# Kernel optimization log

Hardware: AMD Instinct MI355X
Metric: run time of the kernel (lower is better)

Reference implementation:

```python
import jax, jax.numpy as jnp
import numpy as np
import math

N_HEAD = 16

def setup_inputs() -> dict:
    key = jax.random.key(0)
    ks = jax.random.split(key, 8)
    B, S, P, NX = 4, 1024, 128, 1024
    return {
        "x": jax.random.normal(ks[0], (B, S, NX), jnp.float32),
        "M": jax.random.normal(ks[1], (B, P, NX), jnp.float32),
        "Mmask": jnp.ones((B, P), jnp.float32),
        "attention_mask": jnp.zeros((B, 1, 1, S), jnp.float32),
        "W_attn": jax.random.normal(ks[2], (NX, 3 * NX), jnp.float32) * 0.02,
        "b_attn": jnp.zeros((3 * NX,), jnp.float32),
        "W_mem": jax.random.normal(ks[3], (NX, 2 * NX), jnp.float32) * 0.02,
        "b_mem": jnp.zeros((2 * NX,), jnp.float32),
        "W_proj": jax.random.normal(ks[4], (NX, NX), jnp.float32) * 0.02,
        "b_proj": jnp.zeros((NX,), jnp.float32),
    }

def _split_heads(t, H):
    B, T, NX = t.shape
    return t.reshape(B, T, H, NX // H).transpose(0, 2, 1, 3)  # [B,H,T,dh]

def reference(x, M, Mmask, attention_mask, W_attn, b_attn, W_mem, b_mem, W_proj, b_proj):
    B, S, NX = x.shape
    H = N_HEAD
    dh = NX // H
    P = M.shape[1]

    # fused QKV projection (Conv1D == x @ W + b)
    qkv = x @ W_attn + b_attn
    q, k, v = jnp.split(qkv, 3, axis=2)

    # memory K/V projection, prepended along the key/value sequence axis
    ekv = M @ W_mem + b_mem
    ek, ev = jnp.split(ekv, 2, axis=2)
    key = jnp.concatenate([ek, k], axis=1)   # [B, P+S, NX]
    value = jnp.concatenate([ev, v], axis=1)

    qh = _split_heads(q, H)      # [B,H,S,dh]
    kh = _split_heads(key, H)    # [B,H,P+S,dh]
    vh = _split_heads(value, H)  # [B,H,P+S,dh]

    w = jnp.einsum('bhsd,bhtd->bhst', qh, kh) / math.sqrt(dh)  # [B,H,S,P+S]

    # causal bias over the self part, all-ones over the memory part
    causal = jnp.tril(jnp.ones((S, S), w.dtype))
    b = jnp.concatenate([jnp.ones((S, P), w.dtype), causal], axis=1)[None, None]  # [1,1,S,P+S]
    w = w * b - 10000.0 * (1.0 - b)

    # additive attention mask: memory-mask bias concatenated before token mask
    mem_bias = (1.0 - Mmask)[:, None, None, :] * -10000.0  # [B,1,1,P]
    am = jnp.concatenate([mem_bias, jnp.broadcast_to(attention_mask, (B, 1, 1, S))], axis=3)
    w = w + am

    w = jax.nn.softmax(w, axis=-1)
    a = jnp.einsum('bhst,bhtd->bhsd', w, vh)                  # [B,H,S,dh]
    a = a.transpose(0, 2, 1, 3).reshape(B, S, NX)             # merge heads
    return a @ W_proj + b_proj
```

## Files before the change

### kernel.cpp

```cpp
#include <hip/hip_runtime.h>
#include <hip/hip_bf16.h>


typedef __attribute__((ext_vector_type(8))) short bf16x8;
typedef __attribute__((ext_vector_type(4))) float f32x4;

#define MFMA16(a, b, c) __builtin_amdgcn_mfma_f32_16x16x32_bf16((a), (b), (c), 0, 0, 0)

#define GLOAD_LDS16(g, l)                                                  \
    __builtin_amdgcn_global_load_lds(                                      \
        (const __attribute__((address_space(1))) void*)(const void*)(g),   \
        (__attribute__((address_space(3))) void*)(void*)(l), 16, 0, 0)

static __device__ __forceinline__ unsigned short f2bf(float f) {
    union { float f; unsigned int u; } v; v.f = f;
    unsigned int u = v.u;
    return (unsigned short)((u + 0x7fffu + ((u >> 16) & 1u)) >> 16);
}

static __device__ __forceinline__ void transpose64(const float* __restrict__ W,
                                                   unsigned short* __restrict__ Wt,
                                                   int K, int N, int bx, int by,
                                                   float* tile ) {
    const int n0 = bx * 64, k0 = by * 64;
    const int tr = threadIdx.x >> 2, tc = (threadIdx.x & 3) * 16;
    #pragma unroll
    for (int i = 0; i < 4; i++) {
        float4 v = *(const float4*)&W[(size_t)(k0 + tr) * N + n0 + tc + i * 4];
        tile[tr * 65 + tc + i * 4 + 0] = v.x;
        tile[tr * 65 + tc + i * 4 + 1] = v.y;
        tile[tr * 65 + tc + i * 4 + 2] = v.z;
        tile[tr * 65 + tc + i * 4 + 3] = v.w;
    }
    __syncthreads();
    union { ushort4 u4[2]; unsigned short s[8]; } pk[2];
    #pragma unroll
    for (int half = 0; half < 2; half++)
        #pragma unroll
        for (int i = 0; i < 8; i++)
            pk[half].s[i] = f2bf(tile[(tc + half * 8 + i) * 65 + tr]);
    unsigned short* dst = &Wt[(size_t)(n0 + tr) * K + k0 + tc];
    *(ushort4*)(dst + 0) = pk[0].u4[0];
    *(ushort4*)(dst + 4) = pk[0].u4[1];
    *(ushort4*)(dst + 8) = pk[1].u4[0];
    *(ushort4*)(dst + 12) = pk[1].u4[1];
}

__global__ void prep_all(const float* __restrict__ x, const float* __restrict__ Mem,
                         unsigned short* __restrict__ x_bf, unsigned short* __restrict__ M_bf,
                         const float* __restrict__ W_attn, const float* __restrict__ W_mem,
                         const float* __restrict__ W_proj, unsigned short* __restrict__ Wat,
                         unsigned short* __restrict__ Wmt, unsigned short* __restrict__ Wpt,
                         const float* __restrict__ Mmask, const float* __restrict__ amask,
                         float* __restrict__ biasT) {
    __shared__ float tile[64 * 65];
    int bid = blockIdx.x;
    if (bid < 4608) {
        int i = bid * 256 + threadIdx.x;
        if (i < 1048576) {
            float4 v = ((const float4*)x)[i];
            ushort4 o; o.x = f2bf(v.x); o.y = f2bf(v.y); o.z = f2bf(v.z); o.w = f2bf(v.w);
            ((ushort4*)x_bf)[i] = o;
        } else {
            int j = i - 1048576;
            float4 v = ((const float4*)Mem)[j];
            ushort4 o; o.x = f2bf(v.x); o.y = f2bf(v.y); o.z = f2bf(v.z); o.w = f2bf(v.w);
            ((ushort4*)M_bf)[j] = o;
        }
        return;
    }
    bid -= 4608;
    if (bid < 768) {
        transpose64(W_attn, Wat, 1024, 3072, bid % 48, bid / 48, tile);
    } else if (bid < 1280) {
        int t = bid - 768;  transpose64(W_mem, Wmt, 1024, 2048, t % 32, t / 32, tile);
    } else if (bid < 1536) {
        int t = bid - 1280; transpose64(W_proj, Wpt, 1024, 1024, t % 16, t / 16, tile);
    } else {
        int i = (bid - 1536) * 256 + threadIdx.x;
        if (i < 4 * 1152) {
            int b = i / 1152, t = i % 1152;
            float v = (t < 128) ? (Mmask[b * 128 + t] - 1.f) * 10000.f
                                : amask[b * 1024 + t - 128];
            biasT[i] = v * 1.4426950408889634f;
        }
    }
}

__global__ __launch_bounds__(256, 4) void gemm_fused(
        const unsigned short* __restrict__ x_bf, const unsigned short* __restrict__ Wat,
        const float* __restrict__ b_attn, const unsigned short* __restrict__ M_bf,
        const unsigned short* __restrict__ Wmt, const float* __restrict__ b_mem,
        unsigned short* __restrict__ Qbuf, unsigned short* __restrict__ Kc,
        unsigned short* __restrict__ Vt) {
    __shared__ char smem[34816];
    unsigned short* As = (unsigned short*)smem;
    unsigned short* Bs = (unsigned short*)(smem + 8192);
    const int tid = threadIdx.x;
    const int lane = tid & 63, wave = tid >> 6;
    const int quad = lane >> 4, l16 = lane & 15;
    const int crow = lane >> 2, ccol = (lane & 3) * 8;
    const int bid = blockIdx.x;

    if (bid < 768) {
        const int bm = bid & 31, bn = bid >> 5;
        const int wm = (wave & 1) * 64, wn = (wave >> 1) * 64;
        const unsigned short* Abase = x_bf + (size_t)(bm * 128 + crow) * 1024 + ccol;
        const unsigned short* Bbase = Wat + (size_t)(bn * 128 + crow) * 1024 + ccol;
        f32x4 acc[4][4] = {};
        for (int k0 = 0; k0 < 1024; k0 += 32) {
            __syncthreads();
            #pragma unroll
            for (int cc = 0; cc < 4; cc++) {
                const int c = wave * 4 + cc;
                if (c < 8) GLOAD_LDS16(Abase + (size_t)(c * 16) * 1024 + k0, &As[c * 512]);
                else       GLOAD_LDS16(Bbase + (size_t)((c - 8) * 16) * 1024 + k0, &Bs[(c - 8) * 512]);
            }
            __syncthreads();
            bf16x8 af[4], bf[4];
            #pragma unroll
            for (int i = 0; i < 4; i++) af[i] = *(const bf16x8*)&As[(wm + i * 16 + l16) * 32 + quad * 8];
            #pragma unroll
            for (int j = 0; j < 4; j++) bf[j] = *(const bf16x8*)&Bs[(wn + j * 16 + l16) * 32 + quad * 8];
            #pragma unroll
            for (int i = 0; i < 4; i++)
                #pragma unroll
                for (int j = 0; j < 4; j++)
                    acc[i][j] = MFMA16(af[i], bf[j], acc[i][j]);
        }
        float bj[4];
        #pragma unroll
        for (int j = 0; j < 4; j++) bj[j] = b_attn[bn * 128 + wn + j * 16 + l16];
        __syncthreads();
        if (bn < 8) {
            #pragma unroll
            for (int i = 0; i < 4; i++) {
                const int row = bm * 128 + wm + i * 16 + quad * 4;
                #pragma unroll
                for (int j = 0; j < 4; j++) {
                    const int col = bn * 128 + wn + j * 16 + l16;
                    #pragma unroll
                    for (int r = 0; r < 4; r++)
                        Qbuf[(size_t)(row + r) * 1024 + col] = f2bf(acc[i][j][r] + bj[j]);
                }
            }
        } else if (bn < 16) {
            #pragma unroll
            for (int i = 0; i < 4; i++) {
                const int row = bm * 128 + wm + i * 16 + quad * 4;
                const int b = row >> 10, s = row & 1023;
                #pragma unroll
                for (int j = 0; j < 4; j++) {
                    const int c = bn * 128 + wn + j * 16 + l16 - 1024;
                    unsigned short* kd = Kc + (size_t)((b << 4) | (c >> 6)) * 73728 +
                                         (size_t)(s + 128) * 64 + (c & 63);
                    #pragma unroll
                    for (int r = 0; r < 4; r++) kd[(size_t)r * 64] = f2bf(acc[i][j][r] + bj[j]);
                }
            }
        } else {
            unsigned short* Tw = (unsigned short*)smem + wave * 4352;
            #pragma unroll
            for (int i = 0; i < 4; i++)
                #pragma unroll
                for (int j = 0; j < 4; j++)
                    #pragma unroll
                    for (int r = 0; r < 4; r++)
                        Tw[(j * 16 + l16) * 68 + i * 16 + quad * 4 + r] = f2bf(acc[i][j][r] + bj[j]);
            const int vb = (bn - 16) * 128 + wn;
            const int h = vb >> 6;
            const int b = bm >> 3, s0 = (bm * 128 + wm) & 1023;
            unsigned short* vd = Vt + (size_t)((b << 4) | h) * 73728 +
                                 (size_t)lane * 1152 + 128 + s0;
            #pragma unroll
            for (int ch = 0; ch < 8; ch++)
                *(bf16x8*)(vd + ch * 8) = *(const bf16x8*)&Tw[lane * 68 + ch * 8];
        }
    } else {
        const int t = bid - 768;
        const int bm = t >> 5, bn = t & 31;
        const int wm = (wave & 1) * 32, wn = (wave >> 1) * 32;
        const unsigned short* Abase = M_bf + (size_t)(bm * 64 + crow) * 1024 + ccol;
        const unsigned short* Bbase = Wmt + (size_t)(bn * 64 + crow) * 1024 + ccol;
        f32x4 acc[2][2] = {};
        for (int k0 = 0; k0 < 1024; k0 += 32) {
            __syncthreads();
            #pragma unroll
            for (int cc = 0; cc < 2; cc++) {
                const int c = wave * 2 + cc;
                if (c < 4) GLOAD_LDS16(Abase + (size_t)(c * 16) * 1024 + k0, &As[c * 512]);
                else       GLOAD_LDS16(Bbase + (size_t)((c - 4) * 16) * 1024 + k0, &Bs[(c - 4) * 512]);
            }
            __syncthreads();
            bf16x8 af[2], bf[2];
            #pragma unroll
            for (int i = 0; i < 2; i++) af[i] = *(const bf16x8*)&As[(wm + i * 16 + l16) * 32 + quad * 8];
            #pragma unroll
            for (int j = 0; j < 2; j++) bf[j] = *(const bf16x8*)&Bs[(wn + j * 16 + l16) * 32 + quad * 8];
            #pragma unroll
            for (int i = 0; i < 2; i++)
                #pragma unroll
                for (int j = 0; j < 2; j++)
                    acc[i][j] = MFMA16(af[i], bf[j], acc[i][j]);
        }
        float bj[2];
        #pragma unroll
        for (int j = 0; j < 2; j++) bj[j] = b_mem[bn * 64 + wn + j * 16 + l16];
        __syncthreads();
        if (bn < 16) {
            #pragma unroll
            for (int i = 0; i < 2; i++) {
                const int row = bm * 64 + wm + i * 16 + quad * 4;
                const int b = row >> 7, p = row & 127;
                #pragma unroll
                for (int j = 0; j < 2; j++) {
                    const int c = bn * 64 + wn + j * 16 + l16;
                    unsigned short* kd = Kc + (size_t)((b << 4) | (c >> 6)) * 73728 +
                                         (size_t)p * 64 + (c & 63);
                    #pragma unroll
                    for (int r = 0; r < 4; r++) kd[(size_t)r * 64] = f2bf(acc[i][j][r] + bj[j]);
                }
            }
        } else {
            unsigned short* Tw = (unsigned short*)smem + wave * 1152;
            #pragma unroll
            for (int i = 0; i < 2; i++)
                #pragma unroll
                for (int j = 0; j < 2; j++)
                    #pragma unroll
                    for (int r = 0; r < 4; r++)
                        Tw[(j * 16 + l16) * 36 + i * 16 + quad * 4 + r] = f2bf(acc[i][j][r] + bj[j]);
            const int vb = bn * 64 + wn - 1024;
            const int h = vb >> 6, d0 = vb & 63;
            const int b = (bm * 64 + wm) >> 7, p0 = (bm * 64 + wm) & 127;
            const int lc = lane >> 1, half = lane & 1;
            unsigned short* vd = Vt + (size_t)((b << 4) | h) * 73728 +
                                 (size_t)(d0 + lc) * 1152 + p0 + half * 16;
            #pragma unroll
            for (int ch = 0; ch < 2; ch++)
                *(bf16x8*)(vd + ch * 8) = *(const bf16x8*)&Tw[lc * 36 + half * 16 + ch * 8];
        }
    }
}

__global__ __launch_bounds__(128) void attn_kernel(const unsigned short* __restrict__ Qbuf,
                                                   const unsigned short* __restrict__ Kc,
                                                   const unsigned short* __restrict__ Vt,
                                                   const float* __restrict__ biasT,
                                                   unsigned short* __restrict__ Aout) {
    __shared__ unsigned short Ks[64 * 64];
    __shared__ unsigned short Vs[64 * 64];
    __shared__ unsigned short Ps[2][16 * 72];
    const int tid = threadIdx.x;
    const int lane = tid & 63, wave = tid >> 6;
    const int quad = lane >> 4, l16 = lane & 15;
    const int blk = blockIdx.x;
    const int xcd = blk & 7, idx = blk >> 3;
    const int bh = xcd * 8 + (idx & 7);
    const int pair = idx >> 3;
    const int h = bh & 15, b = bh >> 4;

    const unsigned short* Kb = Kc + (size_t)bh * 73728;
    const unsigned short* Vb = Vt + (size_t)bh * 73728;
    const float* bias_b = biasT + b * 1152;

    const int srow = lane >> 3;
    const int scol = ((lane & 7) ^ srow) * 8;
    const int rswz = l16 & 7;
    const int w32 = wave * 32;

    bf16x8 ones;
    #pragma unroll
    for (int j = 0; j < 8; j++) ones[j] = (short)0x3F80;

    #pragma unroll
    for (int phase = 0; phase < 2; phase++) {
        const int qg = phase ? (31 - pair) : pair;
        const int qrow0 = qg * 32;
        const int qrow_w = qrow0 + wave * 16;

        bf16x8 qf[2];
        #pragma unroll
        for (int k2 = 0; k2 < 2; k2++)
            qf[k2] = *(const bf16x8*)(Qbuf + (size_t)(b * 1024 + qrow_w + l16) * 1024 +
                                      h * 64 + k2 * 32 + quad * 8);

        f32x4 o[4] = {};
        f32x4 oden = {};
        const int tmax = min(1152, ((qrow0 + 223) >> 6) << 6);

        for (int t0 = 0; t0 < tmax; t0 += 64) {
            __syncthreads();
            {
                const unsigned short* gk = Kb + (size_t)(t0 + w32 + srow) * 64 + scol;
                const unsigned short* gv = Vb + (size_t)(w32 + srow) * 1152 + t0 + scol;
                #pragma unroll
                for (int cc = 0; cc < 4; cc++) {
                    GLOAD_LDS16(gk + (size_t)(cc * 8) * 64,   &Ks[(w32 + cc * 8) * 64]);
                    GLOAD_LDS16(gv + (size_t)(cc * 8) * 1152, &Vs[(w32 + cc * 8) * 64]);
                }
            }
            __syncthreads();
            if (t0 <= qrow_w + 143) {
                const bool nomask = (t0 + 63 <= 128 + qrow_w);
                float4 bt[4];
                #pragma unroll
                for (int tn = 0; tn < 4; tn++)
                    bt[tn] = *(const float4*)(bias_b + t0 + tn * 16 + quad * 4);
                const int sg = qrow_w + l16;
                #pragma unroll
                for (int tn = 0; tn < 4; tn++) {
                    bf16x8 kf0 = *(const bf16x8*)&Ks[(tn * 16 + l16) * 64 + (quad ^ rswz) * 8];
                    bf16x8 kf1 = *(const bf16x8*)&Ks[(tn * 16 + l16) * 64 + ((quad + 4) ^ rswz) * 8];
                    f32x4 st = {};
                    st = MFMA16(kf0, qf[0], st);
                    st = MFMA16(kf1, qf[1], st);
                    float p[4];
                    #pragma unroll
                    for (int r = 0; r < 4; r++) {
                        float e = __builtin_amdgcn_exp2f(st[r] * 0.18033688011112042f + bt[tn][r]);
                        if (!nomask) {
                            const int tg = t0 + tn * 16 + quad * 4 + r;
                            e = (tg < 128 || tg - 128 <= sg) ? e : 0.f;
                        }
                        p[r] = e;
                    }
                    union { ushort4 u; __hip_bfloat162 h2[2]; } pk;
                    pk.h2[0] = __float22bfloat162_rn(float2{p[0], p[1]});
                    pk.h2[1] = __float22bfloat162_rn(float2{p[2], p[3]});
                    *(ushort4*)&Ps[wave][l16 * 72 + tn * 16 + quad * 4] = pk.u;
                }
                #pragma unroll
                for (int tk = 0; tk < 2; tk++) {
                    bf16x8 pf = *(const bf16x8*)&Ps[wave][l16 * 72 + tk * 32 + quad * 8];
                    oden = MFMA16(pf, ones, oden);
                    #pragma unroll
                    for (int dn = 0; dn < 4; dn++) {
                        bf16x8 vf = *(const bf16x8*)&Vs[(dn * 16 + l16) * 64 +
                                                        ((tk * 4 + quad) ^ rswz) * 8];
                        o[dn] = MFMA16(pf, vf, o[dn]);
                    }
                }
            }
        }

        #pragma unroll
        for (int r = 0; r < 4; r++) {
            const float inv = 1.f / oden[r];
            const size_t orow = (size_t)(b * 1024 + qrow_w + quad * 4 + r) * 1024 + h * 64;
            #pragma unroll
            for (int dn = 0; dn < 4; dn++)
                Aout[orow + dn * 16 + l16] = f2bf(o[dn][r] * inv);
        }
    }
}

__global__ __launch_bounds__(256) void gemm_proj(const unsigned short* __restrict__ Abuf,
                                                 const unsigned short* __restrict__ Wpt,
                                                 const float* __restrict__ b_proj,
                                                 float* __restrict__ out) {
    __shared__ unsigned short As[128 * 32];
    __shared__ unsigned short Bs[64 * 32];
    const int tid = threadIdx.x;
    const int lane = tid & 63, wave = tid >> 6;
    const int quad = lane >> 4, l16 = lane & 15;
    const int wm = (wave & 1) * 64, wn = (wave >> 1) * 32;
    const int bm = blockIdx.x & 31, bn = blockIdx.x >> 5;
    const int crow = lane >> 2, ccol = (lane & 3) * 8;
    const unsigned short* Abase = Abuf + (size_t)(bm * 128 + crow) * 1024 + ccol;
    const unsigned short* Bbase = Wpt + (size_t)(bn * 64 + crow) * 1024 + ccol;

    f32x4 acc[4][2] = {};
    for (int k0 = 0; k0 < 1024; k0 += 32) {
        __syncthreads();
        #pragma unroll
        for (int cc = 0; cc < 3; cc++) {
            const int c = wave * 3 + cc;
            if (c < 8) GLOAD_LDS16(Abase + (size_t)(c * 16) * 1024 + k0, &As[c * 512]);
            else if (c < 12) GLOAD_LDS16(Bbase + (size_t)((c - 8) * 16) * 1024 + k0, &Bs[(c - 8) * 512]);
        }
        __syncthreads();
        bf16x8 af[4], bf[2];
        #pragma unroll
        for (int i = 0; i < 4; i++) af[i] = *(const bf16x8*)&As[(wm + i * 16 + l16) * 32 + quad * 8];
        #pragma unroll
        for (int j = 0; j < 2; j++) bf[j] = *(const bf16x8*)&Bs[(wn + j * 16 + l16) * 32 + quad * 8];
        #pragma unroll
        for (int i = 0; i < 4; i++)
            #pragma unroll
            for (int j = 0; j < 2; j++)
                acc[i][j] = MFMA16(af[i], bf[j], acc[i][j]);
    }
    float bj[2];
    #pragma unroll
    for (int j = 0; j < 2; j++) bj[j] = b_proj[bn * 64 + wn + j * 16 + l16];
    #pragma unroll
    for (int i = 0; i < 4; i++) {
        const int row = bm * 128 + wm + i * 16 + quad * 4;
        #pragma unroll
        for (int j = 0; j < 2; j++) {
            const int col = bn * 64 + wn + j * 16 + l16;
            #pragma unroll
            for (int r = 0; r < 4; r++)
                out[(size_t)(row + r) * 1024 + col] = acc[i][j][r] + bj[j];
        }
    }
}

extern "C" void kernel_launch(void* const* d_in, const int* in_sizes, int n_in,
                              void* d_out, int out_size, void* d_ws, size_t ws_size,
                              hipStream_t stream) {
    const float* x      = (const float*)d_in[0];
    const float* Mem    = (const float*)d_in[1];
    const float* Mmask  = (const float*)d_in[2];
    const float* amask  = (const float*)d_in[3];
    const float* W_attn = (const float*)d_in[4];
    const float* b_attn = (const float*)d_in[5];
    const float* W_mem  = (const float*)d_in[6];
    const float* b_mem  = (const float*)d_in[7];
    const float* W_proj = (const float*)d_in[8];
    const float* b_proj = (const float*)d_in[9];
    float* out = (float*)d_out;

    char* ws = (char*)d_ws;
    unsigned short* x_bf  = (unsigned short*)ws;  ws += (size_t)4096 * 1024 * 2;
    unsigned short* M_bf  = (unsigned short*)ws;  ws += (size_t)512 * 1024 * 2;
    unsigned short* Wat   = (unsigned short*)ws;  ws += (size_t)3072 * 1024 * 2;
    unsigned short* Wmt   = (unsigned short*)ws;  ws += (size_t)2048 * 1024 * 2;
    unsigned short* Wpt   = (unsigned short*)ws;  ws += (size_t)1024 * 1024 * 2;
    unsigned short* Qbuf  = (unsigned short*)ws;  ws += (size_t)4096 * 1024 * 2;
    unsigned short* Abuf  = (unsigned short*)ws;  ws += (size_t)4096 * 1024 * 2;
    unsigned short* Kc    = (unsigned short*)ws;  ws += (size_t)64 * 1152 * 64 * 2;
    unsigned short* Vt    = (unsigned short*)ws;  ws += (size_t)64 * 64 * 1152 * 2;
    float*          biasT = (float*)ws;           ws += (size_t)4 * 1152 * 4;

    prep_all<<<6163, 256, 0, stream>>>(x, Mem, x_bf, M_bf, W_attn, W_mem, W_proj,
                                       Wat, Wmt, Wpt, Mmask, amask, biasT);
    gemm_fused<<<1024, 256, 0, stream>>>(x_bf, Wat, b_attn, M_bf, Wmt, b_mem,
                                         Qbuf, Kc, Vt);
    attn_kernel<<<1024, 128, 0, stream>>>(Qbuf, Kc, Vt, biasT, Abuf);
    gemm_proj<<<512, 256, 0, stream>>>(Abuf, Wpt, b_proj, out);
}
```

Before: 200.6 us.

## Load K/V fragments directly from global memory, dropping LDS staging and barriers

The attention kernel no longer stages K and V tiles in shared memory through global_load_lds with block-wide barriers. Each wave reads its K and V MFMA fragments straight from global memory and runs its own per-wave loop bound. This removes both __syncthreads per tile and the shared K/V buffers, and it lets waves in a block run out of step. The cost is that both waves now fetch the same K/V data separately through the caches with no prefetch, so global latency lands directly on the MFMA chain.

```diff
diff --git a/kernel.cpp b/kernel.cpp
--- a/kernel.cpp
+++ b/kernel.cpp
@@ -248,8 +248,6 @@
                                                    const unsigned short* __restrict__ Vt,
                                                    const float* __restrict__ biasT,
                                                    unsigned short* __restrict__ Aout) {
-    __shared__ unsigned short Ks[64 * 64];
-    __shared__ unsigned short Vs[64 * 64];
     __shared__ unsigned short Ps[2][16 * 72];
     const int tid = threadIdx.x;
     const int lane = tid & 63, wave = tid >> 6;
@@ -264,11 +262,6 @@
     const unsigned short* Vb = Vt + (size_t)bh * 73728;
     const float* bias_b = biasT + b * 1152;
 
-    const int srow = lane >> 3;
-    const int scol = ((lane & 7) ^ srow) * 8;
-    const int rswz = l16 & 7;
-    const int w32 = wave * 32;
-
     bf16x8 ones;
     #pragma unroll
     for (int j = 0; j < 8; j++) ones[j] = (short)0x3F80;
@@ -287,59 +280,47 @@
 
         f32x4 o[4] = {};
         f32x4 oden = {};
-        const int tmax = min(1152, ((qrow0 + 223) >> 6) << 6);
+        const int tmax = min(1152, (((qrow_w + 143) >> 6) << 6) + 64);
+        const int sg = qrow_w + l16;
 
         for (int t0 = 0; t0 < tmax; t0 += 64) {
-            __syncthreads();
-            {
-                const unsigned short* gk = Kb + (size_t)(t0 + w32 + srow) * 64 + scol;
-                const unsigned short* gv = Vb + (size_t)(w32 + srow) * 1152 + t0 + scol;
-                #pragma unroll
-                for (int cc = 0; cc < 4; cc++) {
-                    GLOAD_LDS16(gk + (size_t)(cc * 8) * 64,   &Ks[(w32 + cc * 8) * 64]);
-                    GLOAD_LDS16(gv + (size_t)(cc * 8) * 1152, &Vs[(w32 + cc * 8) * 64]);
+            const bool nomask = (t0 + 63 <= 128 + qrow_w);
+            float4 bt[4];
+            #pragma unroll
+            for (int tn = 0; tn < 4; tn++)
+                bt[tn] = *(const float4*)(bias_b + t0 + tn * 16 + quad * 4);
+            #pragma unroll
+            for (int tn = 0; tn < 4; tn++) {
+                const unsigned short* krow = Kb + (size_t)(t0 + tn * 16 + l16) * 64 + quad * 8;
+                bf16x8 kf0 = *(const bf16x8*)krow;
+                bf16x8 kf1 = *(const bf16x8*)(krow + 32);
+                f32x4 st = {};
+                st = MFMA16(kf0, qf[0], st);
+                st = MFMA16(kf1, qf[1], st);
+                float p[4];
+                #pragma unroll
+                for (int r = 0; r < 4; r++) {
+                    float e = __builtin_amdgcn_exp2f(st[r] * 0.18033688011112042f + bt[tn][r]);
+                    if (!nomask) {
+                        const int tg = t0 + tn * 16 + quad * 4 + r;
+                        e = (tg < 128 || tg - 128 <= sg) ? e : 0.f;
+                    }
+                    p[r] = e;
                 }
-            }
-            __syncthreads();
-            if (t0 <= qrow_w + 143) {
-                const bool nomask = (t0 + 63 <= 128 + qrow_w);
-                float4 bt[4];
-                #pragma unroll
-                for (int tn = 0; tn < 4; tn++)
-                    bt[tn] = *(const float4*)(bias_b + t0 + tn * 16 + quad * 4);
-                const int sg = qrow_w + l16;
-                #pragma unroll
-                for (int tn = 0; tn < 4; tn++) {
-                    bf16x8 kf0 = *(const bf16x8*)&Ks[(tn * 16 + l16) * 64 + (quad ^ rswz) * 8];
-                    bf16x8 kf1 = *(const bf16x8*)&Ks[(tn * 16 + l16) * 64 + ((quad + 4) ^ rswz) * 8];
-                    f32x4 st = {};
-                    st = MFMA16(kf0, qf[0], st);
-                    st = MFMA16(kf1, qf[1], st);
-                    float p[4];
-                    #pragma unroll
-                    for (int r = 0; r < 4; r++) {
-                        float e = __builtin_amdgcn_exp2f(st[r] * 0.18033688011112042f + bt[tn][r]);
-                        if (!nomask) {
-                            const int tg = t0 + tn * 16 + quad * 4 + r;
-                            e = (tg < 128 || tg - 128 <= sg) ? e : 0.f;
-                        }
-                        p[r] = e;
-                    }
-                    union { ushort4 u; __hip_bfloat162 h2[2]; } pk;
-                    pk.h2[0] = __float22bfloat162_rn(float2{p[0], p[1]});
-                    pk.h2[1] = __float22bfloat162_rn(float2{p[2], p[3]});
-                    *(ushort4*)&Ps[wave][l16 * 72 + tn * 16 + quad * 4] = pk.u;
-                }
-                #pragma unroll
-                for (int tk = 0; tk < 2; tk++) {
-                    bf16x8 pf = *(const bf16x8*)&Ps[wave][l16 * 72 + tk * 32 + quad * 8];
-                    oden = MFMA16(pf, ones, oden);
-                    #pragma unroll
-                    for (int dn = 0; dn < 4; dn++) {
-                        bf16x8 vf = *(const bf16x8*)&Vs[(dn * 16 + l16) * 64 +
-                                                        ((tk * 4 + quad) ^ rswz) * 8];
-                        o[dn] = MFMA16(pf, vf, o[dn]);
-                    }
+                union { ushort4 u; __hip_bfloat162 h2[2]; } pk;
+                pk.h2[0] = __float22bfloat162_rn(float2{p[0], p[1]});
+                pk.h2[1] = __float22bfloat162_rn(float2{p[2], p[3]});
+                *(ushort4*)&Ps[wave][l16 * 72 + tn * 16 + quad * 4] = pk.u;
+            }
+            #pragma unroll
+            for (int tk = 0; tk < 2; tk++) {
+                bf16x8 pf = *(const bf16x8*)&Ps[wave][l16 * 72 + tk * 32 + quad * 8];
+                oden = MFMA16(pf, ones, oden);
+                #pragma unroll
+                for (int dn = 0; dn < 4; dn++) {
+                    bf16x8 vf = *(const bf16x8*)(Vb + (size_t)(dn * 16 + l16) * 1152 +
+                                                 t0 + tk * 32 + quad * 8);
+                    o[dn] = MFMA16(pf, vf, o[dn]);
                 }
             }
         }
```

New measurement: 248.6 us. +23.9%, slower.

## Double-buffer K/V tiles in attention kernel to overlap loads with compute

Applied to the files above, without the earlier changes.

The attention kernel now keeps two LDS buffers for the K and V tiles and issues the global-to-LDS loads for the next tile before computing on the current one. Partial vmcnt waits and raw s_barrier instructions replace the paired __syncthreads, so the next tile's loads stay in flight while the current tile is processed. This doubles the K/V shared-memory footprint, which may reduce occupancy. The hand-counted vmcnt(8) must match the number of outstanding loads for the synchronization to stay correct.

```diff
diff --git a/kernel.cpp b/kernel.cpp
--- a/kernel.cpp
+++ b/kernel.cpp
@@ -248,8 +248,8 @@
                                                    const unsigned short* __restrict__ Vt,
                                                    const float* __restrict__ biasT,
                                                    unsigned short* __restrict__ Aout) {
-    __shared__ unsigned short Ks[64 * 64];
-    __shared__ unsigned short Vs[64 * 64];
+    __shared__ unsigned short Ks[2][64 * 64];
+    __shared__ unsigned short Vs[2][64 * 64];
     __shared__ unsigned short Ps[2][16 * 72];
     const int tid = threadIdx.x;
     const int lane = tid & 63, wave = tid >> 6;
@@ -269,6 +269,17 @@
     const int rswz = l16 & 7;
     const int w32 = wave * 32;
 
+#define STAGE_KV(t0_, kdst_, vdst_)                                            \
+    {                                                                          \
+        const unsigned short* gk = Kb + (size_t)((t0_) + w32 + srow) * 64 + scol; \
+        const unsigned short* gv = Vb + (size_t)(w32 + srow) * 1152 + (t0_) + scol; \
+        _Pragma("unroll")                                                      \
+        for (int cc = 0; cc < 4; cc++) {                                       \
+            GLOAD_LDS16(gk + (size_t)(cc * 8) * 64,   &(kdst_)[(w32 + cc * 8) * 64]); \
+            GLOAD_LDS16(gv + (size_t)(cc * 8) * 1152, &(vdst_)[(w32 + cc * 8) * 64]); \
+        }                                                                      \
+    }
+
     bf16x8 ones;
     #pragma unroll
     for (int j = 0; j < 8; j++) ones[j] = (short)0x3F80;
@@ -289,19 +300,20 @@
         f32x4 oden = {};
         const int tmax = min(1152, ((qrow0 + 223) >> 6) << 6);
 
+        STAGE_KV(0, Ks[0], Vs[0]);
+
         for (int t0 = 0; t0 < tmax; t0 += 64) {
-            __syncthreads();
-            {
-                const unsigned short* gk = Kb + (size_t)(t0 + w32 + srow) * 64 + scol;
-                const unsigned short* gv = Vb + (size_t)(w32 + srow) * 1152 + t0 + scol;
-                #pragma unroll
-                for (int cc = 0; cc < 4; cc++) {
-                    GLOAD_LDS16(gk + (size_t)(cc * 8) * 64,   &Ks[(w32 + cc * 8) * 64]);
-                    GLOAD_LDS16(gv + (size_t)(cc * 8) * 1152, &Vs[(w32 + cc * 8) * 64]);
-                }
-            }
-            __syncthreads();
+            const int cur = (t0 >> 6) & 1;
+            if (t0 + 64 < tmax) {
+                if (cur) { STAGE_KV(t0 + 64, Ks[0], Vs[0]); }
+                else     { STAGE_KV(t0 + 64, Ks[1], Vs[1]); }
+                asm volatile("s_waitcnt vmcnt(8)\n\ts_barrier" ::: "memory");
+            } else {
+                asm volatile("s_waitcnt vmcnt(0)\n\ts_barrier" ::: "memory");
+            }
             if (t0 <= qrow_w + 143) {
+                const unsigned short* Kcur = Ks[cur];
+                const unsigned short* Vcur = Vs[cur];
                 const bool nomask = (t0 + 63 <= 128 + qrow_w);
                 float4 bt[4];
                 #pragma unroll
@@ -310,8 +322,8 @@
                 const int sg = qrow_w + l16;
                 #pragma unroll
                 for (int tn = 0; tn < 4; tn++) {
-                    bf16x8 kf0 = *(const bf16x8*)&Ks[(tn * 16 + l16) * 64 + (quad ^ rswz) * 8];
-                    bf16x8 kf1 = *(const bf16x8*)&Ks[(tn * 16 + l16) * 64 + ((quad + 4) ^ rswz) * 8];
+                    bf16x8 kf0 = *(const bf16x8*)&Kcur[(tn * 16 + l16) * 64 + (quad ^ rswz) * 8];
+                    bf16x8 kf1 = *(const bf16x8*)&Kcur[(tn * 16 + l16) * 64 + ((quad + 4) ^ rswz) * 8];
                     f32x4 st = {};
                     st = MFMA16(kf0, qf[0], st);
                     st = MFMA16(kf1, qf[1], st);
@@ -336,12 +348,13 @@
                     oden = MFMA16(pf, ones, oden);
                     #pragma unroll
                     for (int dn = 0; dn < 4; dn++) {
-                        bf16x8 vf = *(const bf16x8*)&Vs[(dn * 16 + l16) * 64 +
-                                                        ((tk * 4 + quad) ^ rswz) * 8];
+                        bf16x8 vf = *(const bf16x8*)&Vcur[(dn * 16 + l16) * 64 +
+                                                          ((tk * 4 + quad) ^ rswz) * 8];
                         o[dn] = MFMA16(pf, vf, o[dn]);
                     }
                 }
             }
+            asm volatile("s_barrier" ::: "memory");
         }
 
         #pragma unroll
@@ -353,6 +366,7 @@
                 Aout[orow + dn * 16 + l16] = f2bf(o[dn][r] * inv);
         }
     }
+#undef STAGE_KV
 }
 
 __global__ __launch_bounds__(256) void gemm_proj(const unsigned short* __restrict__ Abuf,
```

Measured after the change: 198.4 us. Within noise of the previous version (-1.1%).
